# Performance work log

Hardware: AMD Instinct MI355X
Metric: run time of the kernel (lower is better)

The kernel has to match this reference:

```python
import jax, jax.numpy as jnp
import numpy as np
from jax import lax

N = 100000
E = 1600000
IN_C = 128
HID = 128
OUT_C = 64
NUM_CLASSES = 40
BN_EPS = 1e-5


def gcn_conv(x, row, col, W, b):
    # x: [N, F_in] -> [N, F_out]; PyG GCNConv: self-loops + sym normalization
    h = x @ W                                   # [N, F_out]
    loops = jnp.arange(N, dtype=row.dtype)
    r = jnp.concatenate([row, loops])           # [E+N]
    c = jnp.concatenate([col, loops])
    ones = jnp.ones(r.shape[0], dtype=x.dtype)
    deg = jax.ops.segment_sum(ones, c, num_segments=N)
    dinv = jnp.where(deg > 0, lax.rsqrt(deg), jnp.zeros_like(deg))
    norm = dinv[r] * dinv[c]                    # [E+N]
    msg = h[r] * norm[:, None]                  # gather + scale  [E+N, F_out]
    out = jax.ops.segment_sum(msg, c, num_segments=N)
    return out + b


def setup_inputs() -> dict:
    key = jax.random.key(0)
    ks = jax.random.split(key, 16)
    def glorot(k, shape):
        lim = float(np.sqrt(6.0 / (shape[0] + shape[1])))
        return jax.random.uniform(k, shape, jnp.float32, -lim, lim)
    x = jax.random.normal(ks[0], (N, IN_C), jnp.float32)
    edge_index = jax.random.randint(ks[1], (2, E), 0, N, jnp.int64)
    return {
        "x": x,
        "edge_index": edge_index,
        "w1": glorot(ks[2], (IN_C, HID)), "b1": jnp.zeros((HID,), jnp.float32),
        "w2": glorot(ks[3], (HID, HID)), "b2": jnp.zeros((HID,), jnp.float32),
        "bn_gamma": jnp.ones((HID,), jnp.float32), "bn_beta": jnp.zeros((HID,), jnp.float32),
        "bn_mean": jnp.zeros((HID,), jnp.float32), "bn_var": jnp.ones((HID,), jnp.float32),
        "cls_w": glorot(ks[4], (HID, OUT_C)), "cls_b": jnp.zeros((OUT_C,), jnp.float32),
        "sim_w": glorot(ks[5], (HID, NUM_CLASSES)), "sim_b": jnp.zeros((NUM_CLASSES,), jnp.float32),
        "hom_w": glorot(ks[6], (HID, 1)), "hom_b": jnp.zeros((1,), jnp.float32),
        "ent_w": glorot(ks[7], (HID, 1)), "ent_b": jnp.zeros((1,), jnp.float32),
    }


def reference(x, edge_index, w1, b1, w2, b2, bn_gamma, bn_beta, bn_mean, bn_var,
              cls_w, cls_b, sim_w, sim_b, hom_w, hom_b, ent_w, ent_b):
    row, col = edge_index[0], edge_index[1]
    # layer 1: GCNConv -> BN (eval) -> ReLU (dropout is identity in eval)
    h = gcn_conv(x, row, col, w1, b1)
    h = (h - bn_mean) * lax.rsqrt(bn_var + BN_EPS) * bn_gamma + bn_beta
    h = jax.nn.relu(h)
    # layer 2
    h = gcn_conv(h, row, col, w2, b2)
    main_out = jax.nn.log_softmax(h @ cls_w + cls_b, axis=1)
    sim_out = jax.nn.softmax(h @ sim_w + sim_b, axis=1)
    hom_out = jax.nn.sigmoid((h @ hom_w + hom_b)[:, 0])
    ent_out = jax.nn.sigmoid((h @ ent_w + ent_b)[:, 0])
    return (main_out, sim_out, hom_out, ent_out)
```

## Files before the change

kernel.cpp:

```cpp
#include <hip/hip_runtime.h>
#include <hip/hip_bf16.h>
#include <math.h>

#define N_NODES 100000
#define N_EDGES 1600000
#define F 128
#define OUT_C 64
#define NUM_CLASSES 40
#define BN_EPS 1e-5f

#define NBUCK 782
#define BCAP 4096
#define FILL_BLOCKS 512
#define EPB ((N_EDGES + FILL_BLOCKS - 1) / FILL_BLOCKS)

typedef __hip_bfloat16 bf16;
typedef __attribute__((ext_vector_type(8))) short bf16x8;
typedef __attribute__((ext_vector_type(4))) float f32x4;

#define PW1 0
#define PB1 16384
#define PW2 16512
#define PB2 32896
#define PGAMMA 33024
#define PBETA 33152
#define PMEAN 33280
#define PVAR 33408
#define PCLSW 33536
#define PCLSB 41728
#define PSIMW 41792
#define PSIMB 46912
#define PHOMW 46952
#define PHOMB 47080
#define PENTW 47081
#define PENTB 47209
#define PRAW_TOTAL 47210
#define PFW 47232
#define PFB 63616
#define PTOTAL 63744

__device__ __forceinline__ float uasf(unsigned u) { return __uint_as_float(u); }
__device__ __forceinline__ unsigned f2bu(float f) {
    bf16 h = __float2bfloat16(f);
    return (unsigned)*(unsigned short*)&h;
}

__global__ void detect_kernel(const void* __restrict__ x, const void* __restrict__ ei,
                              int* __restrict__ flags) {
    if (blockIdx.x != 0 || threadIdx.x != 0) return;
    const unsigned* xw = (const unsigned*)x;
    int votes = 0;
    for (int i = 0; i < 64; i++) {
        unsigned w = xw[i];
        unsigned e = (w >> 23) & 0xFFu;
        if (w == 0u || (e >= 90u && e <= 160u)) votes++;
    }
    flags[0] = (votes >= 48) ? 1 : 0;
    const unsigned* ew = (const unsigned*)ei;
    int zero_odd = 0;
    for (int i = 0; i < 64; i++)
        if (ew[2 * i + 1] == 0u) zero_odd++;
    flags[1] = (zero_odd >= 60) ? 1 : 0;
}

struct ParamSegs {
    const void* src[16];
    int dst[16];
};

__global__ void cvtparams_kernel(ParamSegs segs, float* __restrict__ params,
                                 const int* __restrict__ flags) {
    int idx = blockIdx.x * 256 + threadIdx.x;
    if (idx >= PRAW_TOTAL) return;
    int k = 0;
#pragma unroll
    for (int s = 1; s < 16; s++)
        if (idx >= segs.dst[s]) k = s;
    int rel = idx - segs.dst[k];
    const void* sp = segs.src[k];
    float v = flags[0] ? ((const float*)sp)[rel]
                       : __bfloat162float(((const bf16*)sp)[rel]);
    params[idx] = v;
}

__device__ __forceinline__ int load_edge(const int* __restrict__ ei, int which, int i, int i64) {
    size_t elem = (size_t)which * N_EDGES + (size_t)i;
    return i64 ? ei[elem * 2] : ei[elem];
}

__global__ __launch_bounds__(256) void fill2_kernel(const int* __restrict__ ei,
                                                    int* __restrict__ bcur,
                                                    int* __restrict__ srcBuck,
                                                    const int* __restrict__ flags) {
    __shared__ int hist[NBUCK];
    __shared__ int gbase[NBUCK];
    __shared__ int lcur[NBUCK];
    int blk = blockIdx.x;
    int t = threadIdx.x;
    int i64 = flags[1];
    int e0 = blk * EPB;
    int ecnt = N_EDGES - e0;
    if (ecnt > EPB) ecnt = EPB;
    for (int i = t; i < NBUCK; i += 256) hist[i] = 0;
    __syncthreads();
    for (int i = t; i < ecnt; i += 256) {
        int c = load_edge(ei, 1, e0 + i, i64);
        atomicAdd(&hist[c >> 7], 1);
    }
    __syncthreads();
    for (int i = t; i < NBUCK; i += 256) {
        int c = hist[i];
        gbase[i] = (c > 0) ? atomicAdd(&bcur[i], c) : 0;
        lcur[i] = 0;
    }
    __syncthreads();
    for (int i = t; i < ecnt; i += 256) {
        int c = load_edge(ei, 1, e0 + i, i64);
        int r = load_edge(ei, 0, e0 + i, i64);
        int b = c >> 7;
        int p = gbase[b] + atomicAdd(&lcur[b], 1);
        if (p < BCAP) srcBuck[b * BCAP + p] = ((c & 127) << 17) | r;
    }
}

__global__ __launch_bounds__(256) void bucketcnt_kernel(const int* __restrict__ srcBuck,
                                                        const int* __restrict__ bcur,
                                                        float* __restrict__ dinv) {
    __shared__ int dcnt[128];
    int b = blockIdx.x;
    int t = threadIdx.x;
    if (t < 128) dcnt[t] = 0;
    __syncthreads();
    int cnt = bcur[b];
    if (cnt > BCAP) cnt = BCAP;
    for (int i = t; i < cnt; i += 256) atomicAdd(&dcnt[srcBuck[b * BCAP + i] >> 17], 1);
    __syncthreads();
    if (t < 128) {
        int n = (b << 7) + t;
        if (n < N_NODES) dinv[n] = rsqrtf((float)(dcnt[t] + 1));
    }
}

__global__ void cvtx_kernel(const void* __restrict__ x, const float* __restrict__ dinv,
                            unsigned short* __restrict__ B16, const int* __restrict__ flags) {
    int i4 = blockIdx.x * blockDim.x + threadIdx.x;
    if (i4 >= N_NODES * F / 4) return;
    int n = i4 >> 5;
    float d = dinv[n];
    float v0, v1, v2, v3;
    if (flags[0]) {
        float4 v = ((const float4*)x)[i4];
        v0 = v.x; v1 = v.y; v2 = v.z; v3 = v.w;
    } else {
        uint2 u = ((const uint2*)x)[i4];
        v0 = uasf(u.x << 16);
        v1 = uasf(u.x & 0xFFFF0000u);
        v2 = uasf(u.y << 16);
        v3 = uasf(u.y & 0xFFFF0000u);
    }
    uint2 o;
    o.x = f2bu(v0 * d) | (f2bu(v1 * d) << 16);
    o.y = f2bu(v2 * d) | (f2bu(v3 * d) << 16);
    ((uint2*)B16)[i4] = o;
}

__device__ __forceinline__ float headw(const float* __restrict__ p, int j, int c) {
    if (c < OUT_C) return p[PCLSW + j * OUT_C + c];
    if (c < OUT_C + NUM_CLASSES) return p[PSIMW + j * NUM_CLASSES + (c - OUT_C)];
    if (c == 104) return p[PHOMW + j];
    if (c == 105) return p[PENTW + j];
    return 0.f;
}

__global__ void fusew_kernel(float* __restrict__ params) {
    int idx = blockIdx.x * 256 + threadIdx.x;
    int k = idx >> 7;
    int c = idx & 127;
    float s = 0.f;
    for (int j = 0; j < 128; j++) s += params[PW2 + k * 128 + j] * headw(params, j, c);
    params[PFW + k * 128 + c] = s;
    if (k == 0) {
        float b = 0.f;
        for (int j = 0; j < 128; j++) b += params[PB2 + j] * headw(params, j, c);
        if (c < OUT_C) b += params[PCLSB + c];
        else if (c < OUT_C + NUM_CLASSES) b += params[PSIMB + c - OUT_C];
        else if (c == 104) b += params[PHOMB];
        else if (c == 105) b += params[PENTB];
        params[PFB + c] = b;
    }
}

__global__ void wcvt_kernel(const float* __restrict__ params, unsigned short* __restrict__ wt) {
    int idx = blockIdx.x * 256 + threadIdx.x;
    if (idx >= 32768) return;
    int which = idx >> 14;
    int local = idx & 16383;
    int n = local >> 7;
    int k = local & 127;
    int ksrc = which ? ((k & 7) * 16 + (k >> 3)) : k;
    float v = params[(which ? PFW : PW1) + ksrc * 128 + n];
    wt[(which << 14) + n * 128 + k] = (unsigned short)f2bu(v);
}

#define ACC8(u)                                \
    do {                                       \
        a[0] += uasf((u).x << 16);             \
        a[1] += uasf((u).x & 0xFFFF0000u);     \
        a[2] += uasf((u).y << 16);             \
        a[3] += uasf((u).y & 0xFFFF0000u);     \
        a[4] += uasf((u).z << 16);             \
        a[5] += uasf((u).z & 0xFFFF0000u);     \
        a[6] += uasf((u).w << 16);             \
        a[7] += uasf((u).w & 0xFFFF0000u);     \
    } while (0)

__global__ __launch_bounds__(512, 8) void agg_kernel(const unsigned short* __restrict__ B16,
                                                     unsigned short* __restrict__ G16,
                                                     const int* __restrict__ srcBuck,
                                                     const int* __restrict__ bcur,
                                                     const float* __restrict__ dinv) {
    __shared__ int raw[BCAP];
    __shared__ int sorted[BCAP];
    __shared__ int dcnt[128], doff[128], dcur[128];
    int b = blockIdx.x;
    int t = threadIdx.x;
    int cnt = bcur[b];
    if (cnt > BCAP) cnt = BCAP;
    if (t < 128) dcnt[t] = 0;
    __syncthreads();
    for (int i = t; i < cnt; i += 512) {
        int e = srcBuck[b * BCAP + i];
        raw[i] = e;
        atomicAdd(&dcnt[e >> 17], 1);
    }
    __syncthreads();
    if (t < 128) doff[t] = dcnt[t];
    __syncthreads();
    for (int d = 1; d < 128; d <<= 1) {
        int add = 0;
        if (t < 128 && t >= d) add = doff[t - d];
        __syncthreads();
        if (t < 128) doff[t] += add;
        __syncthreads();
    }
    if (t < 128) {
        doff[t] -= dcnt[t];
        dcur[t] = 0;
    }
    __syncthreads();
    for (int i = t; i < cnt; i += 512) {
        int e = raw[i];
        int d = e >> 17;
        int r = atomicAdd(&dcur[d], 1);
        sorted[doff[d] + r] = e & 0x1FFFF;
    }
    __syncthreads();

    int g16 = t >> 4;
    int hl8 = (t & 15) << 3;
    int base = b << 7;
    for (int d = g16; d < 128; d += 32) {
        int n = base + d;
        if (n >= N_NODES) break;
        float a[8] = {0.f, 0.f, 0.f, 0.f, 0.f, 0.f, 0.f, 0.f};
        {
            uint4 u = *(const uint4*)(B16 + ((size_t)n << 7) + hl8);
            ACC8(u);
        }
        int o = doff[d], k = dcnt[d];
        int j = 0;
        for (; j + 4 <= k; j += 4) {
            int s0 = sorted[o + j];
            int s1 = sorted[o + j + 1];
            int s2 = sorted[o + j + 2];
            int s3 = sorted[o + j + 3];
            uint4 u0 = *(const uint4*)(B16 + ((size_t)s0 << 7) + hl8);
            uint4 u1 = *(const uint4*)(B16 + ((size_t)s1 << 7) + hl8);
            uint4 u2 = *(const uint4*)(B16 + ((size_t)s2 << 7) + hl8);
            uint4 u3 = *(const uint4*)(B16 + ((size_t)s3 << 7) + hl8);
            ACC8(u0);
            ACC8(u1);
            ACC8(u2);
            ACC8(u3);
        }
        for (; j < k; j++) {
            int s0 = sorted[o + j];
            uint4 u0 = *(const uint4*)(B16 + ((size_t)s0 << 7) + hl8);
            ACC8(u0);
        }
        float dn = dinv[n];
        uint4 pk;
        pk.x = f2bu(a[0] * dn) | (f2bu(a[1] * dn) << 16);
        pk.y = f2bu(a[2] * dn) | (f2bu(a[3] * dn) << 16);
        pk.z = f2bu(a[4] * dn) | (f2bu(a[5] * dn) << 16);
        pk.w = f2bu(a[6] * dn) | (f2bu(a[7] * dn) << 16);
        *(uint4*)(G16 + ((size_t)n << 7) + hl8) = pk;
    }
}

__global__ __launch_bounds__(256) void gemm_mfma_kernel(
    const unsigned short* __restrict__ A16, const unsigned short* __restrict__ Wt,
    unsigned short* __restrict__ outB, void* __restrict__ out,
    const float* __restrict__ params, const float* __restrict__ dinv, int mode,
    const int* __restrict__ flags) {
    __shared__ float sS[128], sO[128], sFB[128];
    int t = threadIdx.x;
    if (t < 128) {
        if (mode) {
            float s = rsqrtf(params[PVAR + t] + BN_EPS) * params[PGAMMA + t];
            sS[t] = s;
            sO[t] = params[PB1 + t] * s + (params[PBETA + t] - params[PMEAN + t] * s);
        } else {
            sFB[t] = params[PFB + t];
        }
    }
    __syncthreads();
    int wave = t >> 6, lane = t & 63, m16 = lane & 15, quad = lane >> 4;
    int rowbase = blockIdx.x * 64 + wave * 16;
    int rA = rowbase + m16;
    if (rA >= N_NODES) rA = N_NODES - 1;
    const size_t abase = (size_t)rA * 128 + (quad << 3);

    f32x4 acc[8];
#pragma unroll
    for (int ct = 0; ct < 8; ct++) acc[ct] = (f32x4){0.f, 0.f, 0.f, 0.f};

#pragma unroll
    for (int kk = 0; kk < 4; kk++) {
        bf16x8 af = *(const bf16x8*)(A16 + abase + kk * 32);
#pragma unroll
        for (int ct = 0; ct < 8; ct++) {
            bf16x8 bf = *(const bf16x8*)(Wt + (size_t)((ct * 16 + m16) * 128) + kk * 32 + (quad << 3));
            acc[ct] = __builtin_amdgcn_mfma_f32_16x16x32_bf16(af, bf, acc[ct], 0, 0, 0);
        }
    }

    int r0 = rowbase + quad * 4;
    if (mode) {
        float sc[8], of[8];
#pragma unroll
        for (int ct = 0; ct < 8; ct++) {
            sc[ct] = sS[ct * 16 + m16];
            of[ct] = sO[ct * 16 + m16];
        }
#pragma unroll
        for (int reg = 0; reg < 4; reg++) {
            int gr = r0 + reg;
            if (gr >= N_NODES) continue;
            float dn = dinv[gr];
            unsigned pk[4];
#pragma unroll
            for (int i = 0; i < 4; i++) {
                float v0 = fmaxf(acc[2 * i][reg] * sc[2 * i] + of[2 * i], 0.f) * dn;
                float v1 = fmaxf(acc[2 * i + 1][reg] * sc[2 * i + 1] + of[2 * i + 1], 0.f) * dn;
                pk[i] = f2bu(v0) | (f2bu(v1) << 16);
            }
            *(uint4*)(outB + (size_t)gr * 128 + (m16 << 3)) = make_uint4(pk[0], pk[1], pk[2], pk[3]);
        }
    } else {
        int isf = flags[0];
        const size_t OFF_SIM = (size_t)N_NODES * OUT_C;
        const size_t OFF_HOM = OFF_SIM + (size_t)N_NODES * NUM_CLASSES;
        const size_t OFF_ENT = OFF_HOM + (size_t)N_NODES;
        float* outf = (float*)out;
        bf16* outb = (bf16*)out;
        float fb[8];
#pragma unroll
        for (int ct = 0; ct < 8; ct++) fb[ct] = sFB[ct * 16 + m16];
#define STORE_OUT(idx, v)                        \
    do {                                         \
        if (isf) outf[(idx)] = (v);              \
        else outb[(idx)] = __float2bfloat16(v);  \
    } while (0)
#pragma unroll
        for (int reg = 0; reg < 4; reg++) {
            int gr = r0 + reg;
            bool vrow = (gr < N_NODES);
            float v[8];
#pragma unroll
            for (int ct = 0; ct < 8; ct++) v[ct] = acc[ct][reg] + fb[ct];
            float m = fmaxf(fmaxf(v[0], v[1]), fmaxf(v[2], v[3]));
            m = fmaxf(m, __shfl_xor(m, 1));
            m = fmaxf(m, __shfl_xor(m, 2));
            m = fmaxf(m, __shfl_xor(m, 4));
            m = fmaxf(m, __shfl_xor(m, 8));
            float S = expf(v[0] - m) + expf(v[1] - m) + expf(v[2] - m) + expf(v[3] - m);
            S += __shfl_xor(S, 1);
            S += __shfl_xor(S, 2);
            S += __shfl_xor(S, 4);
            S += __shfl_xor(S, 8);
            float lS = m + logf(S);
            if (vrow) {
#pragma unroll
                for (int ct = 0; ct < 4; ct++)
                    STORE_OUT((size_t)gr * OUT_C + ct * 16 + m16, v[ct] - lS);
            }
            bool has6 = (m16 < 8);
            float s4 = v[4], s5 = v[5], s6 = has6 ? v[6] : -INFINITY;
            float m2 = fmaxf(fmaxf(s4, s5), s6);
            m2 = fmaxf(m2, __shfl_xor(m2, 1));
            m2 = fmaxf(m2, __shfl_xor(m2, 2));
            m2 = fmaxf(m2, __shfl_xor(m2, 4));
            m2 = fmaxf(m2, __shfl_xor(m2, 8));
            float e4 = expf(s4 - m2), e5 = expf(s5 - m2), e6 = has6 ? expf(s6 - m2) : 0.f;
            float S2 = e4 + e5 + e6;
            S2 += __shfl_xor(S2, 1);
            S2 += __shfl_xor(S2, 2);
            S2 += __shfl_xor(S2, 4);
            S2 += __shfl_xor(S2, 8);
            float rS2 = 1.f / S2;
            if (vrow) {
                STORE_OUT(OFF_SIM + (size_t)gr * NUM_CLASSES + m16, e4 * rS2);
                STORE_OUT(OFF_SIM + (size_t)gr * NUM_CLASSES + 16 + m16, e5 * rS2);
                if (has6) STORE_OUT(OFF_SIM + (size_t)gr * NUM_CLASSES + 32 + m16, e6 * rS2);
                if (m16 == 8) STORE_OUT(OFF_HOM + gr, 1.f / (1.f + expf(-v[6])));
                if (m16 == 9) STORE_OUT(OFF_ENT + gr, 1.f / (1.f + expf(-v[6])));
            }
        }
#undef STORE_OUT
    }
}

extern "C" void kernel_launch(void* const* d_in, const int* in_sizes, int n_in,
                              void* d_out, int out_size, void* d_ws, size_t ws_size,
                              hipStream_t stream) {
    const void* x = d_in[0];
    const int* ei = (const int*)d_in[1];

    char* ws = (char*)d_ws;
    size_t o = 0;
    auto alloc = [&](size_t bytes) {
        size_t r = o;
        o = (o + bytes + 255) & ~(size_t)255;
        return r;
    };
    char* RA = ws + alloc((size_t)51 * 1024 * 1024);
    char* RB = ws + alloc((size_t)26 * 1024 * 1024);
    float* params = (float*)(ws + alloc((size_t)PTOTAL * 4));
    unsigned short* wt = (unsigned short*)(ws + alloc(65536));
    float* dinv = (float*)(ws + alloc((size_t)N_NODES * 4));
    int* bcur = (int*)(ws + alloc((size_t)(NBUCK + 8) * 4));
    int* flags = (int*)(ws + alloc(256));

    int* srcBuck = (int*)RA;
    unsigned short* B16 = (unsigned short*)(RA + 13u * 1024 * 1024);
    unsigned short* G16 = (unsigned short*)RB;

    detect_kernel<<<1, 64, 0, stream>>>(x, ei, flags);
    hipMemsetAsync(bcur, 0, (size_t)(NBUCK + 8) * 4, stream);

    ParamSegs segs;
    const int srcIdx[16] = {2, 3, 4, 5, 6, 7, 8, 9, 10, 11, 12, 13, 14, 15, 16, 17};
    const int dsts[16] = {PW1, PB1, PW2, PB2, PGAMMA, PBETA, PMEAN, PVAR,
                          PCLSW, PCLSB, PSIMW, PSIMB, PHOMW, PHOMB, PENTW, PENTB};
    for (int k = 0; k < 16; k++) {
        segs.src[k] = d_in[srcIdx[k]];
        segs.dst[k] = dsts[k];
    }
    cvtparams_kernel<<<(PRAW_TOTAL + 255) / 256, 256, 0, stream>>>(segs, params, flags);
    fusew_kernel<<<64, 256, 0, stream>>>(params);
    wcvt_kernel<<<128, 256, 0, stream>>>(params, wt);

    fill2_kernel<<<FILL_BLOCKS, 256, 0, stream>>>(ei, bcur, srcBuck, flags);
    bucketcnt_kernel<<<NBUCK, 256, 0, stream>>>(srcBuck, bcur, dinv);
    cvtx_kernel<<<(N_NODES * F / 4 + 255) / 256, 256, 0, stream>>>(x, dinv, B16, flags);

    const int gemmGrid = (N_NODES + 63) / 64;

    agg_kernel<<<NBUCK, 512, 0, stream>>>(B16, G16, srcBuck, bcur, dinv);
    gemm_mfma_kernel<<<gemmGrid, 256, 0, stream>>>(G16, wt, B16, nullptr, params, dinv, 1, flags);
    agg_kernel<<<NBUCK, 512, 0, stream>>>(B16, G16, srcBuck, bcur, dinv);
    gemm_mfma_kernel<<<gemmGrid, 256, 0, stream>>>(G16, wt + 16384, nullptr, d_out, params, dinv, 0, flags);
}
```

Before: 441.5 us.

## Fuse neighbor aggregation with MFMA GEMM through an LDS tile

Merges the aggregation kernel and the following bf16 MFMA GEMM into one kernel per layer. Each 128-node bucket block aggregates its rows into a padded shared-memory tile, which the same block then multiplies by the weights with MFMA. This removes the global write and re-read of the aggregated intermediate and two kernel launches. The cost is a larger LDS footprint, since the tile reuses the raw-edge buffer, and a lower occupancy bound (4 instead of 8), which may hurt the latency-bound gather phase.

```diff
diff --git a/kernel.cpp b/kernel.cpp
--- a/kernel.cpp
+++ b/kernel.cpp
@@ -13,6 +13,8 @@
 #define BCAP 4096
 #define FILL_BLOCKS 512
 #define EPB ((N_EDGES + FILL_BLOCKS - 1) / FILL_BLOCKS)
+
+#define TSTRIDE 136
 
 typedef __hip_bfloat16 bf16;
 typedef __attribute__((ext_vector_type(8))) short bf16x8;
@@ -214,20 +216,36 @@
         a[7] += uasf((u).w & 0xFFFF0000u);     \
     } while (0)
 
-__global__ __launch_bounds__(512, 8) void agg_kernel(const unsigned short* __restrict__ B16,
-                                                     unsigned short* __restrict__ G16,
-                                                     const int* __restrict__ srcBuck,
-                                                     const int* __restrict__ bcur,
-                                                     const float* __restrict__ dinv) {
-    __shared__ int raw[BCAP];
+__global__ __launch_bounds__(512, 4) void aggemm_kernel(
+    const unsigned short* __restrict__ IN16, const unsigned short* __restrict__ Wt,
+    unsigned short* __restrict__ outB, void* __restrict__ out,
+    const float* __restrict__ params, const float* __restrict__ dinv,
+    const int* __restrict__ srcBuck, const int* __restrict__ bcur,
+    int mode, const int* __restrict__ flags) {
     __shared__ int sorted[BCAP];
     __shared__ int dcnt[128], doff[128], dcur[128];
+    __shared__ float sC1[128], sC2[128];
+    __shared__ __align__(16) char scratch[128 * TSTRIDE * 2];
+    int* raw = (int*)scratch;
+    unsigned short* tile = (unsigned short*)scratch;
+
     int b = blockIdx.x;
     int t = threadIdx.x;
+
+    if (t < 128) {
+        if (mode) {
+            float s = rsqrtf(params[PVAR + t] + BN_EPS) * params[PGAMMA + t];
+            sC1[t] = s;
+            sC2[t] = params[PB1 + t] * s + (params[PBETA + t] - params[PMEAN + t] * s);
+        } else {
+            sC1[t] = params[PFB + t];
+        }
+        dcnt[t] = 0;
+    }
+    __syncthreads();
+
     int cnt = bcur[b];
     if (cnt > BCAP) cnt = BCAP;
-    if (t < 128) dcnt[t] = 0;
-    __syncthreads();
     for (int i = t; i < cnt; i += 512) {
         int e = srcBuck[b * BCAP + i];
         raw[i] = e;
@@ -261,65 +279,46 @@
     int base = b << 7;
     for (int d = g16; d < 128; d += 32) {
         int n = base + d;
-        if (n >= N_NODES) break;
-        float a[8] = {0.f, 0.f, 0.f, 0.f, 0.f, 0.f, 0.f, 0.f};
-        {
-            uint4 u = *(const uint4*)(B16 + ((size_t)n << 7) + hl8);
-            ACC8(u);
-        }
-        int o = doff[d], k = dcnt[d];
-        int j = 0;
-        for (; j + 4 <= k; j += 4) {
-            int s0 = sorted[o + j];
-            int s1 = sorted[o + j + 1];
-            int s2 = sorted[o + j + 2];
-            int s3 = sorted[o + j + 3];
-            uint4 u0 = *(const uint4*)(B16 + ((size_t)s0 << 7) + hl8);
-            uint4 u1 = *(const uint4*)(B16 + ((size_t)s1 << 7) + hl8);
-            uint4 u2 = *(const uint4*)(B16 + ((size_t)s2 << 7) + hl8);
-            uint4 u3 = *(const uint4*)(B16 + ((size_t)s3 << 7) + hl8);
-            ACC8(u0);
-            ACC8(u1);
-            ACC8(u2);
-            ACC8(u3);
-        }
-        for (; j < k; j++) {
-            int s0 = sorted[o + j];
-            uint4 u0 = *(const uint4*)(B16 + ((size_t)s0 << 7) + hl8);
-            ACC8(u0);
-        }
-        float dn = dinv[n];
-        uint4 pk;
-        pk.x = f2bu(a[0] * dn) | (f2bu(a[1] * dn) << 16);
-        pk.y = f2bu(a[2] * dn) | (f2bu(a[3] * dn) << 16);
-        pk.z = f2bu(a[4] * dn) | (f2bu(a[5] * dn) << 16);
-        pk.w = f2bu(a[6] * dn) | (f2bu(a[7] * dn) << 16);
-        *(uint4*)(G16 + ((size_t)n << 7) + hl8) = pk;
-    }
-}
-
-__global__ __launch_bounds__(256) void gemm_mfma_kernel(
-    const unsigned short* __restrict__ A16, const unsigned short* __restrict__ Wt,
-    unsigned short* __restrict__ outB, void* __restrict__ out,
-    const float* __restrict__ params, const float* __restrict__ dinv, int mode,
-    const int* __restrict__ flags) {
-    __shared__ float sS[128], sO[128], sFB[128];
-    int t = threadIdx.x;
-    if (t < 128) {
-        if (mode) {
-            float s = rsqrtf(params[PVAR + t] + BN_EPS) * params[PGAMMA + t];
-            sS[t] = s;
-            sO[t] = params[PB1 + t] * s + (params[PBETA + t] - params[PMEAN + t] * s);
-        } else {
-            sFB[t] = params[PFB + t];
-        }
-    }
-    __syncthreads();
-    int wave = t >> 6, lane = t & 63, m16 = lane & 15, quad = lane >> 4;
-    int rowbase = blockIdx.x * 64 + wave * 16;
-    int rA = rowbase + m16;
-    if (rA >= N_NODES) rA = N_NODES - 1;
-    const size_t abase = (size_t)rA * 128 + (quad << 3);
+        uint4 pk = make_uint4(0u, 0u, 0u, 0u);
+        if (n < N_NODES) {
+            float a[8] = {0.f, 0.f, 0.f, 0.f, 0.f, 0.f, 0.f, 0.f};
+            {
+                uint4 u = *(const uint4*)(IN16 + ((size_t)n << 7) + hl8);
+                ACC8(u);
+            }
+            int o = doff[d], k = dcnt[d];
+            int j = 0;
+            for (; j + 4 <= k; j += 4) {
+                int s0 = sorted[o + j];
+                int s1 = sorted[o + j + 1];
+                int s2 = sorted[o + j + 2];
+                int s3 = sorted[o + j + 3];
+                uint4 u0 = *(const uint4*)(IN16 + ((size_t)s0 << 7) + hl8);
+                uint4 u1 = *(const uint4*)(IN16 + ((size_t)s1 << 7) + hl8);
+                uint4 u2 = *(const uint4*)(IN16 + ((size_t)s2 << 7) + hl8);
+                uint4 u3 = *(const uint4*)(IN16 + ((size_t)s3 << 7) + hl8);
+                ACC8(u0);
+                ACC8(u1);
+                ACC8(u2);
+                ACC8(u3);
+            }
+            for (; j < k; j++) {
+                int s0 = sorted[o + j];
+                uint4 u0 = *(const uint4*)(IN16 + ((size_t)s0 << 7) + hl8);
+                ACC8(u0);
+            }
+            float dn = dinv[n];
+            pk.x = f2bu(a[0] * dn) | (f2bu(a[1] * dn) << 16);
+            pk.y = f2bu(a[2] * dn) | (f2bu(a[3] * dn) << 16);
+            pk.z = f2bu(a[4] * dn) | (f2bu(a[5] * dn) << 16);
+            pk.w = f2bu(a[6] * dn) | (f2bu(a[7] * dn) << 16);
+        }
+        *(uint4*)((char*)tile + (size_t)d * (TSTRIDE * 2) + (hl8 << 1)) = pk;
+    }
+    __syncthreads();
+
+    int w = t >> 6, lane = t & 63, m16 = lane & 15, quad = lane >> 4;
+    int rloc = w * 16 + m16;
 
     f32x4 acc[8];
 #pragma unroll
@@ -327,21 +326,22 @@
 
 #pragma unroll
     for (int kk = 0; kk < 4; kk++) {
-        bf16x8 af = *(const bf16x8*)(A16 + abase + kk * 32);
+        bf16x8 af = *(const bf16x8*)((char*)tile + (size_t)rloc * (TSTRIDE * 2) + kk * 64 + quad * 16);
 #pragma unroll
         for (int ct = 0; ct < 8; ct++) {
-            bf16x8 bf = *(const bf16x8*)(Wt + (size_t)((ct * 16 + m16) * 128) + kk * 32 + (quad << 3));
-            acc[ct] = __builtin_amdgcn_mfma_f32_16x16x32_bf16(af, bf, acc[ct], 0, 0, 0);
-        }
-    }
-
+            bf16x8 bfr = *(const bf16x8*)(Wt + (size_t)((ct * 16 + m16) * 128) + kk * 32 + (quad << 3));
+            acc[ct] = __builtin_amdgcn_mfma_f32_16x16x32_bf16(af, bfr, acc[ct], 0, 0, 0);
+        }
+    }
+
+    int rowbase = base + w * 16;
     int r0 = rowbase + quad * 4;
     if (mode) {
         float sc[8], of[8];
 #pragma unroll
         for (int ct = 0; ct < 8; ct++) {
-            sc[ct] = sS[ct * 16 + m16];
-            of[ct] = sO[ct * 16 + m16];
+            sc[ct] = sC1[ct * 16 + m16];
+            of[ct] = sC2[ct * 16 + m16];
         }
 #pragma unroll
         for (int reg = 0; reg < 4; reg++) {
@@ -366,7 +366,7 @@
         bf16* outb = (bf16*)out;
         float fb[8];
 #pragma unroll
-        for (int ct = 0; ct < 8; ct++) fb[ct] = sFB[ct * 16 + m16];
+        for (int ct = 0; ct < 8; ct++) fb[ct] = sC1[ct * 16 + m16];
 #define STORE_OUT(idx, v)                        \
     do {                                         \
         if (isf) outf[(idx)] = (v);              \
@@ -465,10 +465,8 @@
     bucketcnt_kernel<<<NBUCK, 256, 0, stream>>>(srcBuck, bcur, dinv);
     cvtx_kernel<<<(N_NODES * F / 4 + 255) / 256, 256, 0, stream>>>(x, dinv, B16, flags);
 
-    const int gemmGrid = (N_NODES + 63) / 64;
-
-    agg_kernel<<<NBUCK, 512, 0, stream>>>(B16, G16, srcBuck, bcur, dinv);
-    gemm_mfma_kernel<<<gemmGrid, 256, 0, stream>>>(G16, wt, B16, nullptr, params, dinv, 1, flags);
-    agg_kernel<<<NBUCK, 512, 0, stream>>>(B16, G16, srcBuck, bcur, dinv);
-    gemm_mfma_kernel<<<gemmGrid, 256, 0, stream>>>(G16, wt + 16384, nullptr, d_out, params, dinv, 0, flags);
-}
+    aggemm_kernel<<<NBUCK, 512, 0, stream>>>(B16, wt, G16, nullptr, params, dinv,
+                                             srcBuck, bcur, 1, flags);
+    aggemm_kernel<<<NBUCK, 512, 0, stream>>>(G16, wt + 16384, nullptr, d_out, params, dinv,
+                                             srcBuck, bcur, 0, flags);
+}
```

Result: faster. 431.7 us (-2.2%).

## Presort edge buckets once and split aggregation by feature half per XCC

Applied to the files above, without the earlier changes.

The per-destination counting sort moves out of both aggregation kernels into a single presort kernel that writes the sorted sources, offsets and counts to global memory. Aggregation now runs as twice as many blocks, each handling one 64-feature half of a bucket. Work is handed out through atomic counters keyed on the XCC id, so each half of the feature matrix tends to stay in one group of caches. Smaller changes: fill caches destination indices in registers instead of reloading them, detect uses wave ballots, and softmax/log uses fast intrinsics. The costs are extra global index reads per aggregation and slightly less accurate exp/log.

```diff
diff --git a/kernel.cpp b/kernel.cpp
--- a/kernel.cpp
+++ b/kernel.cpp
@@ -13,6 +13,7 @@
 #define BCAP 4096
 #define FILL_BLOCKS 512
 #define EPB ((N_EDGES + FILL_BLOCKS - 1) / FILL_BLOCKS)
+#define FILL_ITERS 13
 
 typedef __hip_bfloat16 bf16;
 typedef __attribute__((ext_vector_type(8))) short bf16x8;
@@ -47,20 +48,20 @@
 
 __global__ void detect_kernel(const void* __restrict__ x, const void* __restrict__ ei,
                               int* __restrict__ flags) {
-    if (blockIdx.x != 0 || threadIdx.x != 0) return;
+    if (blockIdx.x != 0) return;
+    int t = threadIdx.x & 63;
     const unsigned* xw = (const unsigned*)x;
-    int votes = 0;
-    for (int i = 0; i < 64; i++) {
-        unsigned w = xw[i];
-        unsigned e = (w >> 23) & 0xFFu;
-        if (w == 0u || (e >= 90u && e <= 160u)) votes++;
-    }
-    flags[0] = (votes >= 48) ? 1 : 0;
+    unsigned w = xw[t];
+    unsigned e = (w >> 23) & 0xFFu;
+    bool vote = (w == 0u || (e >= 90u && e <= 160u));
+    unsigned long long m1 = __ballot(vote);
     const unsigned* ew = (const unsigned*)ei;
-    int zero_odd = 0;
-    for (int i = 0; i < 64; i++)
-        if (ew[2 * i + 1] == 0u) zero_odd++;
-    flags[1] = (zero_odd >= 60) ? 1 : 0;
+    bool zo = (ew[2 * t + 1] == 0u);
+    unsigned long long m2 = __ballot(zo);
+    if (t == 0) {
+        flags[0] = (__popcll(m1) >= 48) ? 1 : 0;
+        flags[1] = (__popcll(m2) >= 60) ? 1 : 0;
+    }
 }
 
 struct ParamSegs {
@@ -103,9 +104,16 @@
     if (ecnt > EPB) ecnt = EPB;
     for (int i = t; i < NBUCK; i += 256) hist[i] = 0;
     __syncthreads();
-    for (int i = t; i < ecnt; i += 256) {
-        int c = load_edge(ei, 1, e0 + i, i64);
-        atomicAdd(&hist[c >> 7], 1);
+    int ccache[FILL_ITERS];
+#pragma unroll
+    for (int it = 0; it < FILL_ITERS; ++it) {
+        int i = t + it * 256;
+        int c = -1;
+        if (i < ecnt) {
+            c = load_edge(ei, 1, e0 + i, i64);
+            atomicAdd(&hist[c >> 7], 1);
+        }
+        ccache[it] = c;
     }
     __syncthreads();
     for (int i = t; i < NBUCK; i += 256) {
@@ -114,28 +122,64 @@
         lcur[i] = 0;
     }
     __syncthreads();
-    for (int i = t; i < ecnt; i += 256) {
-        int c = load_edge(ei, 1, e0 + i, i64);
-        int r = load_edge(ei, 0, e0 + i, i64);
-        int b = c >> 7;
-        int p = gbase[b] + atomicAdd(&lcur[b], 1);
-        if (p < BCAP) srcBuck[b * BCAP + p] = ((c & 127) << 17) | r;
-    }
-}
-
-__global__ __launch_bounds__(256) void bucketcnt_kernel(const int* __restrict__ srcBuck,
-                                                        const int* __restrict__ bcur,
-                                                        float* __restrict__ dinv) {
-    __shared__ int dcnt[128];
+#pragma unroll
+    for (int it = 0; it < FILL_ITERS; ++it) {
+        int i = t + it * 256;
+        if (i < ecnt) {
+            int c = ccache[it];
+            int r = load_edge(ei, 0, e0 + i, i64);
+            int b = c >> 7;
+            int p = gbase[b] + atomicAdd(&lcur[b], 1);
+            if (p < BCAP) srcBuck[b * BCAP + p] = ((c & 127) << 17) | r;
+        }
+    }
+}
+
+__global__ __launch_bounds__(512) void presort_kernel(int* __restrict__ srcBuck,
+                                                      const int* __restrict__ bcur,
+                                                      int* __restrict__ doffG,
+                                                      int* __restrict__ dcntG,
+                                                      float* __restrict__ dinv) {
+    __shared__ int raw[BCAP];
+    __shared__ int sorted[BCAP];
+    __shared__ int dcnt[128], doff[128], dcur[128];
     int b = blockIdx.x;
     int t = threadIdx.x;
-    if (t < 128) dcnt[t] = 0;
-    __syncthreads();
     int cnt = bcur[b];
     if (cnt > BCAP) cnt = BCAP;
-    for (int i = t; i < cnt; i += 256) atomicAdd(&dcnt[srcBuck[b * BCAP + i] >> 17], 1);
-    __syncthreads();
+    if (t < 128) dcnt[t] = 0;
+    __syncthreads();
+    for (int i = t; i < cnt; i += 512) {
+        int e = srcBuck[b * BCAP + i];
+        raw[i] = e;
+        atomicAdd(&dcnt[e >> 17], 1);
+    }
+    __syncthreads();
+    if (t < 128) doff[t] = dcnt[t];
+    __syncthreads();
+    for (int d = 1; d < 128; d <<= 1) {
+        int add = 0;
+        if (t < 128 && t >= d) add = doff[t - d];
+        __syncthreads();
+        if (t < 128) doff[t] += add;
+        __syncthreads();
+    }
     if (t < 128) {
+        doff[t] -= dcnt[t];
+        dcur[t] = 0;
+    }
+    __syncthreads();
+    for (int i = t; i < cnt; i += 512) {
+        int e = raw[i];
+        int d = e >> 17;
+        int r = atomicAdd(&dcur[d], 1);
+        sorted[doff[d] + r] = e & 0x1FFFF;
+    }
+    __syncthreads();
+    for (int i = t; i < cnt; i += 512) srcBuck[b * BCAP + i] = sorted[i];
+    if (t < 128) {
+        doffG[(b << 7) + t] = doff[t];
+        dcntG[(b << 7) + t] = dcnt[t];
         int n = (b << 7) + t;
         if (n < N_NODES) dinv[n] = rsqrtf((float)(dcnt[t] + 1));
     }
@@ -202,100 +246,79 @@
     wt[(which << 14) + n * 128 + k] = (unsigned short)f2bu(v);
 }
 
-#define ACC8(u)                                \
-    do {                                       \
-        a[0] += uasf((u).x << 16);             \
-        a[1] += uasf((u).x & 0xFFFF0000u);     \
-        a[2] += uasf((u).y << 16);             \
-        a[3] += uasf((u).y & 0xFFFF0000u);     \
-        a[4] += uasf((u).z << 16);             \
-        a[5] += uasf((u).z & 0xFFFF0000u);     \
-        a[6] += uasf((u).w << 16);             \
-        a[7] += uasf((u).w & 0xFFFF0000u);     \
+__global__ __launch_bounds__(512) void aggh_kernel(const unsigned short* __restrict__ IN16,
+                                                   unsigned short* __restrict__ OUT16,
+                                                   const int* __restrict__ srcBuck,
+                                                   const int* __restrict__ doffG,
+                                                   const int* __restrict__ dcntG,
+                                                   const float* __restrict__ dinv,
+                                                   int* __restrict__ wcnt) {
+    __shared__ int sb, sh;
+    int t = threadIdx.x;
+    if (t == 0) {
+        unsigned xcc;
+        asm volatile("s_getreg_b32 %0, hwreg(HW_REG_XCC_ID)" : "=s"(xcc));
+        int half = (xcc >> 2) & 1;
+        int idx = atomicAdd(&wcnt[half], 1);
+        if (idx >= NBUCK) {
+            half ^= 1;
+            idx = atomicAdd(&wcnt[half], 1);
+        }
+        sb = idx;
+        sh = half;
+    }
+    __syncthreads();
+    int b = sb, h = sh;
+    if (b >= NBUCK) return;
+
+    int g16 = t >> 4;
+    int f4 = (t & 15) << 2;
+    size_t hoff = (size_t)(h * 64 + f4);
+    int base = b << 7;
+
+#define ACC4(u)                               \
+    do {                                      \
+        a0 += uasf((u).x << 16);              \
+        a1 += uasf((u).x & 0xFFFF0000u);      \
+        a2 += uasf((u).y << 16);              \
+        a3 += uasf((u).y & 0xFFFF0000u);      \
     } while (0)
 
-__global__ __launch_bounds__(512, 8) void agg_kernel(const unsigned short* __restrict__ B16,
-                                                     unsigned short* __restrict__ G16,
-                                                     const int* __restrict__ srcBuck,
-                                                     const int* __restrict__ bcur,
-                                                     const float* __restrict__ dinv) {
-    __shared__ int raw[BCAP];
-    __shared__ int sorted[BCAP];
-    __shared__ int dcnt[128], doff[128], dcur[128];
-    int b = blockIdx.x;
-    int t = threadIdx.x;
-    int cnt = bcur[b];
-    if (cnt > BCAP) cnt = BCAP;
-    if (t < 128) dcnt[t] = 0;
-    __syncthreads();
-    for (int i = t; i < cnt; i += 512) {
-        int e = srcBuck[b * BCAP + i];
-        raw[i] = e;
-        atomicAdd(&dcnt[e >> 17], 1);
-    }
-    __syncthreads();
-    if (t < 128) doff[t] = dcnt[t];
-    __syncthreads();
-    for (int d = 1; d < 128; d <<= 1) {
-        int add = 0;
-        if (t < 128 && t >= d) add = doff[t - d];
-        __syncthreads();
-        if (t < 128) doff[t] += add;
-        __syncthreads();
-    }
-    if (t < 128) {
-        doff[t] -= dcnt[t];
-        dcur[t] = 0;
-    }
-    __syncthreads();
-    for (int i = t; i < cnt; i += 512) {
-        int e = raw[i];
-        int d = e >> 17;
-        int r = atomicAdd(&dcur[d], 1);
-        sorted[doff[d] + r] = e & 0x1FFFF;
-    }
-    __syncthreads();
-
-    int g16 = t >> 4;
-    int hl8 = (t & 15) << 3;
-    int base = b << 7;
     for (int d = g16; d < 128; d += 32) {
         int n = base + d;
         if (n >= N_NODES) break;
-        float a[8] = {0.f, 0.f, 0.f, 0.f, 0.f, 0.f, 0.f, 0.f};
+        float a0 = 0.f, a1 = 0.f, a2 = 0.f, a3 = 0.f;
         {
-            uint4 u = *(const uint4*)(B16 + ((size_t)n << 7) + hl8);
-            ACC8(u);
-        }
-        int o = doff[d], k = dcnt[d];
+            uint2 u = *(const uint2*)(IN16 + ((size_t)n << 7) + hoff);
+            ACC4(u);
+        }
+        int o = doffG[(b << 7) + d];
+        int k = dcntG[(b << 7) + d];
+        const int* sp = srcBuck + b * BCAP + o;
         int j = 0;
         for (; j + 4 <= k; j += 4) {
-            int s0 = sorted[o + j];
-            int s1 = sorted[o + j + 1];
-            int s2 = sorted[o + j + 2];
-            int s3 = sorted[o + j + 3];
-            uint4 u0 = *(const uint4*)(B16 + ((size_t)s0 << 7) + hl8);
-            uint4 u1 = *(const uint4*)(B16 + ((size_t)s1 << 7) + hl8);
-            uint4 u2 = *(const uint4*)(B16 + ((size_t)s2 << 7) + hl8);
-            uint4 u3 = *(const uint4*)(B16 + ((size_t)s3 << 7) + hl8);
-            ACC8(u0);
-            ACC8(u1);
-            ACC8(u2);
-            ACC8(u3);
+            int s0 = sp[j], s1 = sp[j + 1], s2 = sp[j + 2], s3 = sp[j + 3];
+            uint2 u0 = *(const uint2*)(IN16 + ((size_t)s0 << 7) + hoff);
+            uint2 u1 = *(const uint2*)(IN16 + ((size_t)s1 << 7) + hoff);
+            uint2 u2 = *(const uint2*)(IN16 + ((size_t)s2 << 7) + hoff);
+            uint2 u3 = *(const uint2*)(IN16 + ((size_t)s3 << 7) + hoff);
+            ACC4(u0);
+            ACC4(u1);
+            ACC4(u2);
+            ACC4(u3);
         }
         for (; j < k; j++) {
-            int s0 = sorted[o + j];
-            uint4 u0 = *(const uint4*)(B16 + ((size_t)s0 << 7) + hl8);
-            ACC8(u0);
+            int s0 = sp[j];
+            uint2 u0 = *(const uint2*)(IN16 + ((size_t)s0 << 7) + hoff);
+            ACC4(u0);
         }
         float dn = dinv[n];
-        uint4 pk;
-        pk.x = f2bu(a[0] * dn) | (f2bu(a[1] * dn) << 16);
-        pk.y = f2bu(a[2] * dn) | (f2bu(a[3] * dn) << 16);
-        pk.z = f2bu(a[4] * dn) | (f2bu(a[5] * dn) << 16);
-        pk.w = f2bu(a[6] * dn) | (f2bu(a[7] * dn) << 16);
-        *(uint4*)(G16 + ((size_t)n << 7) + hl8) = pk;
-    }
+        uint2 pk;
+        pk.x = f2bu(a0 * dn) | (f2bu(a1 * dn) << 16);
+        pk.y = f2bu(a2 * dn) | (f2bu(a3 * dn) << 16);
+        *(uint2*)(OUT16 + ((size_t)n << 7) + hoff) = pk;
+    }
+#undef ACC4
 }
 
 __global__ __launch_bounds__(256) void gemm_mfma_kernel(
@@ -330,8 +353,8 @@
         bf16x8 af = *(const bf16x8*)(A16 + abase + kk * 32);
 #pragma unroll
         for (int ct = 0; ct < 8; ct++) {
-            bf16x8 bf = *(const bf16x8*)(Wt + (size_t)((ct * 16 + m16) * 128) + kk * 32 + (quad << 3));
-            acc[ct] = __builtin_amdgcn_mfma_f32_16x16x32_bf16(af, bf, acc[ct], 0, 0, 0);
+            bf16x8 bfr = *(const bf16x8*)(Wt + (size_t)((ct * 16 + m16) * 128) + kk * 32 + (quad << 3));
+            acc[ct] = __builtin_amdgcn_mfma_f32_16x16x32_bf16(af, bfr, acc[ct], 0, 0, 0);
         }
     }
 
@@ -384,12 +407,12 @@
             m = fmaxf(m, __shfl_xor(m, 2));
             m = fmaxf(m, __shfl_xor(m, 4));
             m = fmaxf(m, __shfl_xor(m, 8));
-            float S = expf(v[0] - m) + expf(v[1] - m) + expf(v[2] - m) + expf(v[3] - m);
+            float S = __expf(v[0] - m) + __expf(v[1] - m) + __expf(v[2] - m) + __expf(v[3] - m);
             S += __shfl_xor(S, 1);
             S += __shfl_xor(S, 2);
             S += __shfl_xor(S, 4);
             S += __shfl_xor(S, 8);
-            float lS = m + logf(S);
+            float lS = m + __logf(S);
             if (vrow) {
 #pragma unroll
                 for (int ct = 0; ct < 4; ct++)
@@ -402,7 +425,7 @@
             m2 = fmaxf(m2, __shfl_xor(m2, 2));
             m2 = fmaxf(m2, __shfl_xor(m2, 4));
             m2 = fmaxf(m2, __shfl_xor(m2, 8));
-            float e4 = expf(s4 - m2), e5 = expf(s5 - m2), e6 = has6 ? expf(s6 - m2) : 0.f;
+            float e4 = __expf(s4 - m2), e5 = __expf(s5 - m2), e6 = has6 ? __expf(s6 - m2) : 0.f;
             float S2 = e4 + e5 + e6;
             S2 += __shfl_xor(S2, 1);
             S2 += __shfl_xor(S2, 2);
@@ -413,8 +436,8 @@
                 STORE_OUT(OFF_SIM + (size_t)gr * NUM_CLASSES + m16, e4 * rS2);
                 STORE_OUT(OFF_SIM + (size_t)gr * NUM_CLASSES + 16 + m16, e5 * rS2);
                 if (has6) STORE_OUT(OFF_SIM + (size_t)gr * NUM_CLASSES + 32 + m16, e6 * rS2);
-                if (m16 == 8) STORE_OUT(OFF_HOM + gr, 1.f / (1.f + expf(-v[6])));
-                if (m16 == 9) STORE_OUT(OFF_ENT + gr, 1.f / (1.f + expf(-v[6])));
+                if (m16 == 8) STORE_OUT(OFF_HOM + gr, 1.f / (1.f + __expf(-v[6])));
+                if (m16 == 9) STORE_OUT(OFF_ENT + gr, 1.f / (1.f + __expf(-v[6])));
             }
         }
 #undef STORE_OUT
@@ -439,7 +462,10 @@
     float* params = (float*)(ws + alloc((size_t)PTOTAL * 4));
     unsigned short* wt = (unsigned short*)(ws + alloc(65536));
     float* dinv = (float*)(ws + alloc((size_t)N_NODES * 4));
+    int* doffG = (int*)(ws + alloc((size_t)NBUCK * 128 * 4));
+    int* dcntG = (int*)(ws + alloc((size_t)NBUCK * 128 * 4));
     int* bcur = (int*)(ws + alloc((size_t)(NBUCK + 8) * 4));
+    int* wcnt = (int*)(ws + alloc(256));
     int* flags = (int*)(ws + alloc(256));
 
     int* srcBuck = (int*)RA;
@@ -447,7 +473,7 @@
     unsigned short* G16 = (unsigned short*)RB;
 
     detect_kernel<<<1, 64, 0, stream>>>(x, ei, flags);
-    hipMemsetAsync(bcur, 0, (size_t)(NBUCK + 8) * 4, stream);
+    hipMemsetAsync(bcur, 0, (size_t)((char*)wcnt + 256 - (char*)bcur), stream);
 
     ParamSegs segs;
     const int srcIdx[16] = {2, 3, 4, 5, 6, 7, 8, 9, 10, 11, 12, 13, 14, 15, 16, 17};
@@ -462,13 +488,13 @@
     wcvt_kernel<<<128, 256, 0, stream>>>(params, wt);
 
     fill2_kernel<<<FILL_BLOCKS, 256, 0, stream>>>(ei, bcur, srcBuck, flags);
-    bucketcnt_kernel<<<NBUCK, 256, 0, stream>>>(srcBuck, bcur, dinv);
+    presort_kernel<<<NBUCK, 512, 0, stream>>>(srcBuck, bcur, doffG, dcntG, dinv);
     cvtx_kernel<<<(N_NODES * F / 4 + 255) / 256, 256, 0, stream>>>(x, dinv, B16, flags);
 
     const int gemmGrid = (N_NODES + 63) / 64;
 
-    agg_kernel<<<NBUCK, 512, 0, stream>>>(B16, G16, srcBuck, bcur, dinv);
+    aggh_kernel<<<2 * NBUCK, 512, 0, stream>>>(B16, G16, srcBuck, doffG, dcntG, dinv, wcnt);
     gemm_mfma_kernel<<<gemmGrid, 256, 0, stream>>>(G16, wt, B16, nullptr, params, dinv, 1, flags);
-    agg_kernel<<<NBUCK, 512, 0, stream>>>(B16, G16, srcBuck, bcur, dinv);
+    aggh_kernel<<<2 * NBUCK, 512, 0, stream>>>(B16, G16, srcBuck, doffG, dcntG, dinv, wcnt + 2);
     gemm_mfma_kernel<<<gemmGrid, 256, 0, stream>>>(G16, wt + 16384, nullptr, d_out, params, dinv, 0, flags);
 }
```

Result: slower. 463.8 us (+5.1%).
